# Kernel tuning notes

Hardware: AMD Instinct MI355X
Metric: run time of the kernel (lower is better)

Reference implementation:

```python
import jax, jax.numpy as jnp
import numpy as np

B, N, IN_C = 8, 2048, 256
HEADS, OUT_C = 4, 128
E = 65536
BN_EPS = 1e-5


def setup_inputs() -> dict:
    key = jax.random.key(0)
    k1, k2, k3, k4 = jax.random.split(key, 4)
    x = jax.random.normal(k1, (B, N, IN_C), dtype=jnp.float32)
    edge_index = jax.random.randint(k2, (2, E), 0, N, dtype=jnp.int64)
    # Linear W: in_channels -> heads*out_channels, no bias (stored as [in, out])
    W = jax.random.normal(k3, (IN_C, HEADS * OUT_C), dtype=jnp.float32) / np.sqrt(IN_C)
    # att Linear: 2*out_channels -> 1, no bias (stored as a vector)
    a = jax.random.normal(k4, (2 * OUT_C,), dtype=jnp.float32) / np.sqrt(2 * OUT_C)
    bn_gamma = jnp.ones((OUT_C,), dtype=jnp.float32)
    bn_beta = jnp.zeros((OUT_C,), dtype=jnp.float32)
    return {"x": x, "edge_index": edge_index, "W": W, "a": a,
            "bn_gamma": bn_gamma, "bn_beta": bn_beta}


def reference(x, edge_index, W, a, bn_gamma, bn_beta):
    Bsz, Nn, _ = x.shape
    src, dst = edge_index[0], edge_index[1]
    h = (x @ W).reshape(Bsz, Nn, HEADS, OUT_C)  # [B,N,H,C]
    # att([h_src, h_dst]) == h_src @ a[:C] + h_dst @ a[C:] ; precompute per node
    s_src = jnp.einsum("bnhc,c->bnh", h, a[:OUT_C])  # [B,N,H]
    s_dst = jnp.einsum("bnhc,c->bnh", h, a[OUT_C:])
    e = s_src[:, src] + s_dst[:, dst]                 # [B,E,H]
    e = jax.nn.leaky_relu(e, negative_slope=0.2)
    e_avg = e.mean(axis=-1)                           # [B,E]
    # dense N x N attention: rows = dst, cols = src, -inf elsewhere
    attn = jnp.full((Bsz, Nn, Nn), -jnp.inf, dtype=x.dtype)
    attn = attn.at[:, dst, src].set(e_avg)
    attn = jax.nn.softmax(attn, axis=-1)
    attn = jnp.nan_to_num(attn, nan=0.0)              # rows with no edges -> 0
    # dropout is identity in eval mode
    h_flat = h.reshape(Bsz, Nn, HEADS * OUT_C)
    h_out = attn @ h_flat                             # [B,N,H*C]
    h_out = h_out.reshape(Bsz, Nn, HEADS, OUT_C).mean(axis=2)  # [B,N,C]
    # BatchNorm1d over channel dim (batch stats, biased var, affine params)
    mean = h_out.mean(axis=(0, 1))
    var = h_out.var(axis=(0, 1))
    h_out = (h_out - mean) / jnp.sqrt(var + BN_EPS) * bn_gamma + bn_beta
    return jax.nn.elu(h_out)
```

## Files before the change

kernel.cpp:

```cpp
#include <hip/hip_runtime.h>
#include <hip/hip_bf16.h>
#include <math.h>

#define BB 8
#define NN 2048
#define INC 256
#define CC 128
#define NE 65536
#define CAP 128
#define MROWS (BB*NN)
#define BN_EPS 1e-5f
#define NT 9
#define NKC 8
#define NFRAG (NT*NKC*64)
#define FPSCALE 4194304.0

typedef unsigned int uint32;
typedef unsigned long long u64;
typedef __attribute__((ext_vector_type(8))) short short8;
typedef __attribute__((ext_vector_type(4))) float f32x4;

__device__ inline ushort f2bf(float f) {
  __hip_bfloat16 b = __float2bfloat16(f);
  return reinterpret_cast<ushort&>(b);
}
__device__ inline float bf2f(ushort h) {
  return __uint_as_float(((uint32)h) << 16);
}

__device__ inline void load_edge(const void* ei, int is64, int e, int& s, int& d) {
  if (is64) {
    const long long* p = (const long long*)ei;
    s = (int)p[e]; d = (int)p[NE + e];
  } else {
    const int* p = (const int*)ei;
    s = p[e]; d = p[NE + e];
  }
}

__global__ __launch_bounds__(256) void k_prep(const float* __restrict__ W,
                                              const float* __restrict__ a,
                                              const int* __restrict__ ei32,
                                              uint4* __restrict__ pack,
                                              int* __restrict__ flag,
                                              int* __restrict__ row_cnt,
                                              u64* __restrict__ bins) {
  __shared__ float Wl[8][520];
  __shared__ float Wms[8][132];
  __shared__ float Was[8][8];
  __shared__ float av[256];
  int m = blockIdx.x, tid = threadIdx.x;
  if (m < 8) row_cnt[m * 256 + tid] = 0;
  if (m == 8) {
    #pragma unroll
    for (int i = 0; i < 8; ++i) bins[tid * 8 + i] = 0ull;
  }
  if (m == 0 && tid == 0) {
    int nz = 0;
    for (int t = 1; t < 128; t += 2) nz |= (ei32[t] != 0);
    *flag = nz ? 0 : 1;
  }
  av[tid] = a[tid];
  const float4* Wg = (const float4*)(W + (size_t)m * 8 * 512);
  #pragma unroll
  for (int i = 0; i < 4; ++i) {
    int idx = tid + i * 256;
    int r = idx >> 7, c4 = idx & 127;
    *(float4*)&Wl[r][c4 * 4] = Wg[idx];
  }
  __syncthreads();
  {
    int c = tid & 127, half = tid >> 7;
    #pragma unroll
    for (int ii = 0; ii < 4; ++ii) {
      int r = half * 4 + ii;
      Wms[r][c] = 0.25f * (Wl[r][c] + Wl[r][128 + c] + Wl[r][256 + c] + Wl[r][384 + c]);
    }
  }
  {
    int i8 = tid >> 5, c2 = tid & 31;
    float p[8];
    #pragma unroll
    for (int j = 0; j < 8; ++j) p[j] = 0.0f;
    #pragma unroll
    for (int t4 = 0; t4 < 4; ++t4) {
      int cc = c2 + t4 * 32;
      float asrc = av[cc], adst = av[128 + cc];
      #pragma unroll
      for (int h = 0; h < 4; ++h) {
        float w = Wl[i8][h * 128 + cc];
        p[h] += w * asrc;
        p[4 + h] += w * adst;
      }
    }
    #pragma unroll
    for (int off = 16; off > 0; off >>= 1)
      #pragma unroll
      for (int j = 0; j < 8; ++j) p[j] += __shfl_xor(p[j], off, 64);
    if (c2 < 8) Was[i8][c2] = p[c2];
  }
  __syncthreads();
  if (tid < 144) {
    int t = tid >> 4, l16 = tid & 15;
    int cch = t * 16 + l16;
    int kc = m >> 2, g = m & 3;
    uint32 h[8];
    #pragma unroll
    for (int j = 0; j < 8; ++j) {
      float v = 0.0f;
      if (cch < CC) v = Wms[j][cch];
      else if (cch < CC + 8) v = Was[j][cch - CC];
      h[j] = (uint32)f2bf(v);
    }
    uint4 u;
    u.x = h[0] | (h[1] << 16);
    u.y = h[2] | (h[3] << 16);
    u.z = h[4] | (h[5] << 16);
    u.w = h[6] | (h[7] << 16);
    pack[(t * NKC + kc) * 64 + g * 16 + l16] = u;
  }
}

__global__ __launch_bounds__(512) void k_gemm(const float* __restrict__ x,
                                              const uint4* __restrict__ pack,
                                              const void* __restrict__ ei,
                                              const int* __restrict__ flag,
                                              ushort* __restrict__ hm,
                                              float* __restrict__ s,
                                              int* __restrict__ row_cnt,
                                              int* __restrict__ row_src) {
  __shared__ uint4 lp[NFRAG];
  int tid = threadIdx.x;
  if (tid < 256) {
    int e = blockIdx.x * 256 + tid;
    int is64 = *flag;
    int src, dst;
    load_edge(ei, is64, e, src, dst);
    int pos = atomicAdd(&row_cnt[dst], 1);
    if (pos < CAP) row_src[dst * CAP + pos] = src;
  }
  #pragma unroll
  for (int i = 0; i < 9; ++i) lp[i * 512 + tid] = pack[i * 512 + tid];

  int lane = tid & 63, wv = tid >> 6;
  int rt = wv & 3, th = wv >> 2;
  int g = lane >> 4;
  int xrow = blockIdx.x * 64 + rt * 16 + (lane & 15);
  const float* xr = x + (size_t)xrow * INC;

  short8 xf[8];
  #pragma unroll
  for (int kc = 0; kc < 8; ++kc) {
    f32x4 xa = *(const f32x4*)(xr + kc * 32 + g * 8);
    f32x4 xb = *(const f32x4*)(xr + kc * 32 + g * 8 + 4);
    short8 t;
    t[0] = (short)f2bf(xa[0]); t[1] = (short)f2bf(xa[1]);
    t[2] = (short)f2bf(xa[2]); t[3] = (short)f2bf(xa[3]);
    t[4] = (short)f2bf(xb[0]); t[5] = (short)f2bf(xb[1]);
    t[6] = (short)f2bf(xb[2]); t[7] = (short)f2bf(xb[3]);
    xf[kc] = t;
  }
  __syncthreads();

  f32x4 acc[4];
  f32x4 accE = (f32x4)(0.0f);
  #pragma unroll
  for (int i = 0; i < 4; ++i) acc[i] = (f32x4)(0.0f);

  const short8* fr = (const short8*)lp;
  int tb = th * 4;
  #pragma unroll
  for (int kc = 0; kc < NKC; ++kc) {
    #pragma unroll
    for (int i = 0; i < 4; ++i) {
      short8 af = fr[((tb + i) * NKC + kc) * 64 + lane];
      acc[i] = __builtin_amdgcn_mfma_f32_16x16x32_bf16(af, xf[kc], acc[i], 0, 0, 0);
    }
    short8 ae = fr[(8 * NKC + kc) * 64 + lane];
    accE = __builtin_amdgcn_mfma_f32_16x16x32_bf16(ae, xf[kc], accE, 0, 0, 0);
  }

  ushort* hrow = hm + (size_t)xrow * CC;
  #pragma unroll
  for (int i = 0; i < 4; ++i) {
    int t = tb + i;
    uint32 p0 = (uint32)f2bf(acc[i][0]) | ((uint32)f2bf(acc[i][1]) << 16);
    uint32 p1 = (uint32)f2bf(acc[i][2]) | ((uint32)f2bf(acc[i][3]) << 16);
    *(uint2*)(hrow + t * 16 + g * 4) = make_uint2(p0, p1);
  }
  if (th == 1 && g < 2) {
    *(f32x4*)(s + (size_t)xrow * 8 + g * 4) = accE;
  }
}

__device__ inline float edge_e(f32x4 ss, f32x4 sd) {
  float sum = 0.0f;
  #pragma unroll
  for (int h = 0; h < 4; ++h) {
    float v = ss[h] + sd[h];
    sum += (v > 0.0f) ? v : 0.2f * v;
  }
  return 0.25f * sum;
}

__global__ __launch_bounds__(256) void k_agg(const int* __restrict__ row_cnt,
                                             const int* __restrict__ row_src,
                                             const float* __restrict__ s,
                                             const uint32* __restrict__ hm32,
                                             uint32* __restrict__ hout,
                                             u64* __restrict__ bins) {
  __shared__ int rsrc[CAP], csrc[CAP];
  __shared__ float swgt[8][CAP];
  __shared__ f32x4 red[256];
  __shared__ uint32 bmask[64];
  __shared__ int wcnt[2];
  int d = blockIdx.x, tid = threadIdx.x;
  int lane = tid & 63, wv = tid >> 6;
  int k0 = row_cnt[d]; if (k0 > CAP) k0 = CAP;

  if (tid < 64) bmask[tid] = 0u;
  if (tid < k0) rsrc[tid] = row_src[d * CAP + tid];
  __syncthreads();
  int keep = 0;
  if (tid < k0) {
    int sv = rsrc[tid];
    uint32 bit = 1u << (sv & 31);
    uint32 old = atomicOr(&bmask[sv >> 5], bit);
    keep = ((old & bit) == 0) ? 1 : 0;
  }
  u64 mask = __ballot(keep);
  int pos = __popcll(mask & ((1ull << lane) - 1ull));
  if (lane == 0 && wv < 2) wcnt[wv] = (int)__popcll(mask);
  __syncthreads();
  int base = (wv == 1) ? wcnt[0] : 0;
  if (keep) csrc[base + pos] = rsrc[tid];
  __syncthreads();
  int kd = wcnt[0] + wcnt[1];
  if (tid < kd) {
    int sv = csrc[tid], r = 0;
    for (int q = 0; q < kd; ++q) r += (csrc[q] < sv) ? 1 : 0;
    rsrc[r] = sv;
  }
  __syncthreads();

  int b0 = wv, b1 = wv + 4;
  const float* sb0 = s + (size_t)b0 * NN * 8;
  const float* sb1 = s + (size_t)b1 * NN * 8;
  f32x4 sd0 = *(const f32x4*)(sb0 + (size_t)d * 8 + 4);
  f32x4 sd1 = *(const f32x4*)(sb1 + (size_t)d * 8 + 4);
  float v00 = -INFINITY, v01 = -INFINITY, v10 = -INFINITY, v11 = -INFINITY;
  if (lane < kd) {
    int r = rsrc[lane];
    f32x4 s0 = *(const f32x4*)(sb0 + (size_t)r * 8);
    f32x4 s1 = *(const f32x4*)(sb1 + (size_t)r * 8);
    v00 = edge_e(s0, sd0);
    v10 = edge_e(s1, sd1);
  }
  if (lane + 64 < kd) {
    int r = rsrc[lane + 64];
    f32x4 s0 = *(const f32x4*)(sb0 + (size_t)r * 8);
    f32x4 s1 = *(const f32x4*)(sb1 + (size_t)r * 8);
    v01 = edge_e(s0, sd0);
    v11 = edge_e(s1, sd1);
  }
  float m0 = fmaxf(v00, v01), m1 = fmaxf(v10, v11);
  #pragma unroll
  for (int off = 32; off > 0; off >>= 1) {
    m0 = fmaxf(m0, __shfl_xor(m0, off, 64));
    m1 = fmaxf(m1, __shfl_xor(m1, off, 64));
  }
  float e00 = (lane < kd)      ? expf(v00 - m0) : 0.0f;
  float e01 = (lane + 64 < kd) ? expf(v01 - m0) : 0.0f;
  float e10 = (lane < kd)      ? expf(v10 - m1) : 0.0f;
  float e11 = (lane + 64 < kd) ? expf(v11 - m1) : 0.0f;
  float sum0 = e00 + e01, sum1 = e10 + e11;
  #pragma unroll
  for (int off = 32; off > 0; off >>= 1) {
    sum0 += __shfl_xor(sum0, off, 64);
    sum1 += __shfl_xor(sum1, off, 64);
  }
  float inv0 = (kd > 0) ? 1.0f / sum0 : 0.0f;
  float inv1 = (kd > 0) ? 1.0f / sum1 : 0.0f;
  swgt[b0][lane]      = e00 * inv0;
  swgt[b0][lane + 64] = e01 * inv0;
  swgt[b1][lane]      = e10 * inv1;
  swgt[b1][lane + 64] = e11 * inv1;

  float a0 = 0.0f, a1 = 0.0f, a2 = 0.0f, a3 = 0.0f;
  const uint32* hb0 = hm32 + (size_t)b0 * NN * (CC / 2);
  const uint32* hb1 = hm32 + (size_t)b1 * NN * (CC / 2);
  #pragma unroll 4
  for (int j = 0; j < kd; ++j) {
    int r = rsrc[j];
    float w0 = swgt[b0][j], w1 = swgt[b1][j];
    uint32 u0 = hb0[(size_t)r * (CC / 2) + lane];
    uint32 u1 = hb1[(size_t)r * (CC / 2) + lane];
    a0 += w0 * bf2f((ushort)(u0 & 0xffffu));
    a1 += w0 * bf2f((ushort)(u0 >> 16));
    a2 += w1 * bf2f((ushort)(u1 & 0xffffu));
    a3 += w1 * bf2f((ushort)(u1 >> 16));
  }
  hout[((size_t)b0 * NN + d) * (CC / 2) + lane] =
      (uint32)f2bf(a0) | ((uint32)f2bf(a1) << 16);
  hout[((size_t)b1 * NN + d) * (CC / 2) + lane] =
      (uint32)f2bf(a2) | ((uint32)f2bf(a3) << 16);

  f32x4 r4;
  r4[0] = a0 + a2; r4[1] = a0 * a0 + a2 * a2;
  r4[2] = a1 + a3; r4[3] = a1 * a1 + a3 * a3;
  red[tid] = r4;
  __syncthreads();
  if (wv == 0) {
    f32x4 t = red[lane] + red[lane + 64] + red[lane + 128] + red[lane + 192];
    u64* bb = bins + (size_t)(d & 7) * (CC * 2);
    atomicAdd(&bb[4 * lane + 0], (u64)(long long)llrint((double)t[0] * FPSCALE));
    atomicAdd(&bb[4 * lane + 1], (u64)(long long)llrint((double)t[1] * FPSCALE));
    atomicAdd(&bb[4 * lane + 2], (u64)(long long)llrint((double)t[2] * FPSCALE));
    atomicAdd(&bb[4 * lane + 3], (u64)(long long)llrint((double)t[3] * FPSCALE));
  }
}

__global__ __launch_bounds__(256) void k_elu(const uint32* __restrict__ hout,
                                             const u64* __restrict__ bins,
                                             const float* __restrict__ gamma,
                                             const float* __restrict__ beta,
                                             float* __restrict__ out) {
  __shared__ float bsc[CC], bsh[CC];
  int tid = threadIdx.x;
  if (tid < CC) {
    long long S = 0, Q = 0;
    #pragma unroll
    for (int bin = 0; bin < 8; ++bin) {
      S += (long long)bins[bin * (CC * 2) + 2 * tid];
      Q += (long long)bins[bin * (CC * 2) + 2 * tid + 1];
    }
    double mean = (double)S / FPSCALE / (double)MROWS;
    double var  = (double)Q / FPSCALE / (double)MROWS - mean * mean;
    if (var < 0.0) var = 0.0;
    float scale = gamma[tid] / sqrtf((float)var + BN_EPS);
    bsc[tid] = scale;
    bsh[tid] = beta[tid] - (float)mean * scale;
  }
  __syncthreads();
  int pbase = blockIdx.x * 1024 + tid;
  #pragma unroll
  for (int i = 0; i < 4; ++i) {
    int p = pbase + i * 256;
    int cp = p & 63;
    uint32 u = hout[p];
    float y0 = bf2f((ushort)(u & 0xffffu)) * bsc[2 * cp]     + bsh[2 * cp];
    float y1 = bf2f((ushort)(u >> 16))     * bsc[2 * cp + 1] + bsh[2 * cp + 1];
    float2 o;
    o.x = (y0 > 0.0f) ? y0 : expm1f(y0);
    o.y = (y1 > 0.0f) ? y1 : expm1f(y1);
    *(float2*)(out + 2 * (size_t)p) = o;
  }
}

extern "C" void kernel_launch(void* const* d_in, const int* in_sizes, int n_in,
                              void* d_out, int out_size, void* d_ws, size_t ws_size,
                              hipStream_t stream) {
  const float* x     = (const float*)d_in[0];
  const void*  ei    = d_in[1];
  const float* W     = (const float*)d_in[2];
  const float* a     = (const float*)d_in[3];
  const float* gamma = (const float*)d_in[4];
  const float* beta  = (const float*)d_in[5];
  float* out = (float*)d_out;

  char* p = (char*)d_ws;
  ushort* hm   = (ushort*)p; p += (size_t)MROWS * CC * 2;
  uint32* hout = (uint32*)p; p += (size_t)MROWS * CC * 2;
  float* s    = (float*)p; p += (size_t)MROWS * 8 * 4;
  uint4* pack = (uint4*)p; p += (size_t)NFRAG * 16;
  u64* bins   = (u64*)p;   p += 8 * CC * 2 * 8;
  int* flag   = (int*)p;   p += 256;
  int* row_cnt  = (int*)p; p += NN * 4;
  int* row_src  = (int*)p; p += (size_t)NN * CAP * 4;

  k_prep<<<32, 256, 0, stream>>>(W, a, (const int*)ei, pack, flag, row_cnt, bins);
  k_gemm<<<MROWS / 64, 512, 0, stream>>>(x, pack, ei, flag, hm, s, row_cnt, row_src);
  k_agg<<<NN, 256, 0, stream>>>(row_cnt, row_src, s, (const uint32*)hm, hout, bins);
  k_elu<<<(MROWS * CC / 2) / 1024, 256, 0, stream>>>(hout, bins, gamma, beta, out);
}
```

Before: 63.32 us.

## Interleave batch pairs in projected features for wider gathers and packed FMA

The GEMM now writes its bf16 output so that batch b and batch b+4 share the same node row, stored as interleaved 32-bit words. The aggregation kernel can then fetch both batches' features for a neighbour with one 8-byte load per lane instead of two 4-byte loads. It also stores the two batches' softmax weights as a float2 pair and accumulates with two-wide float vectors, which can map to packed FMA instructions. The cost is strided 32-bit stores in the GEMM epilogue instead of contiguous 8-byte stores, and correctness depends on the aggregation's wave-to-batch mapping being b0=wv, b1=wv+4.

```diff
diff --git a/kernel.cpp b/kernel.cpp
--- a/kernel.cpp
+++ b/kernel.cpp
@@ -19,6 +19,7 @@
 typedef unsigned long long u64;
 typedef __attribute__((ext_vector_type(8))) short short8;
 typedef __attribute__((ext_vector_type(4))) float f32x4;
+typedef __attribute__((ext_vector_type(2))) float f32x2;
 
 __device__ inline ushort f2bf(float f) {
   __hip_bfloat16 b = __float2bfloat16(f);
@@ -125,7 +126,7 @@
                                               const uint4* __restrict__ pack,
                                               const void* __restrict__ ei,
                                               const int* __restrict__ flag,
-                                              ushort* __restrict__ hm,
+                                              uint32* __restrict__ hm32,
                                               float* __restrict__ s,
                                               int* __restrict__ row_cnt,
                                               int* __restrict__ row_src) {
@@ -180,13 +181,16 @@
     accE = __builtin_amdgcn_mfma_f32_16x16x32_bf16(ae, xf[kc], accE, 0, 0, 0);
   }
 
-  ushort* hrow = hm + (size_t)xrow * CC;
+  int b = xrow >> 11, n = xrow & (NN - 1);
+  int pp = b & 3, hh = b >> 2;
+  uint32* hbase = hm32 + ((size_t)pp * NN + n) * 128 + hh;
   #pragma unroll
   for (int i = 0; i < 4; ++i) {
     int t = tb + i;
     uint32 p0 = (uint32)f2bf(acc[i][0]) | ((uint32)f2bf(acc[i][1]) << 16);
     uint32 p1 = (uint32)f2bf(acc[i][2]) | ((uint32)f2bf(acc[i][3]) << 16);
-    *(uint2*)(hrow + t * 16 + g * 4) = make_uint2(p0, p1);
+    hbase[(t * 8 + g * 2) * 2]     = p0;
+    hbase[(t * 8 + g * 2 + 1) * 2] = p1;
   }
   if (th == 1 && g < 2) {
     *(f32x4*)(s + (size_t)xrow * 8 + g * 4) = accE;
@@ -206,11 +210,11 @@
 __global__ __launch_bounds__(256) void k_agg(const int* __restrict__ row_cnt,
                                              const int* __restrict__ row_src,
                                              const float* __restrict__ s,
-                                             const uint32* __restrict__ hm32,
+                                             const uint2* __restrict__ hm2,
                                              uint32* __restrict__ hout,
                                              u64* __restrict__ bins) {
   __shared__ int rsrc[CAP], csrc[CAP];
-  __shared__ float swgt[8][CAP];
+  __shared__ float2 swp[4][CAP];
   __shared__ f32x4 red[256];
   __shared__ uint32 bmask[64];
   __shared__ int wcnt[2];
@@ -281,33 +285,33 @@
   }
   float inv0 = (kd > 0) ? 1.0f / sum0 : 0.0f;
   float inv1 = (kd > 0) ? 1.0f / sum1 : 0.0f;
-  swgt[b0][lane]      = e00 * inv0;
-  swgt[b0][lane + 64] = e01 * inv0;
-  swgt[b1][lane]      = e10 * inv1;
-  swgt[b1][lane + 64] = e11 * inv1;
-
-  float a0 = 0.0f, a1 = 0.0f, a2 = 0.0f, a3 = 0.0f;
-  const uint32* hb0 = hm32 + (size_t)b0 * NN * (CC / 2);
-  const uint32* hb1 = hm32 + (size_t)b1 * NN * (CC / 2);
-  #pragma unroll 4
+  swp[wv][lane]      = make_float2(e00 * inv0, e10 * inv1);
+  swp[wv][lane + 64] = make_float2(e01 * inv0, e11 * inv1);
+
+  f32x2 a01 = (f32x2)(0.0f);
+  f32x2 a23 = (f32x2)(0.0f);
+  const uint2* hp = hm2 + (size_t)wv * NN * 64 + lane;
+  #pragma unroll 8
   for (int j = 0; j < kd; ++j) {
     int r = rsrc[j];
-    float w0 = swgt[b0][j], w1 = swgt[b1][j];
-    uint32 u0 = hb0[(size_t)r * (CC / 2) + lane];
-    uint32 u1 = hb1[(size_t)r * (CC / 2) + lane];
-    a0 += w0 * bf2f((ushort)(u0 & 0xffffu));
-    a1 += w0 * bf2f((ushort)(u0 >> 16));
-    a2 += w1 * bf2f((ushort)(u1 & 0xffffu));
-    a3 += w1 * bf2f((ushort)(u1 >> 16));
+    float2 w = swp[wv][j];
+    uint2 u = hp[(size_t)r * 64];
+    f32x2 h0, h1;
+    h0[0] = __uint_as_float(u.x << 16);
+    h0[1] = __uint_as_float(u.x & 0xffff0000u);
+    h1[0] = __uint_as_float(u.y << 16);
+    h1[1] = __uint_as_float(u.y & 0xffff0000u);
+    a01 += h0 * w.x;
+    a23 += h1 * w.y;
   }
   hout[((size_t)b0 * NN + d) * (CC / 2) + lane] =
-      (uint32)f2bf(a0) | ((uint32)f2bf(a1) << 16);
+      (uint32)f2bf(a01[0]) | ((uint32)f2bf(a01[1]) << 16);
   hout[((size_t)b1 * NN + d) * (CC / 2) + lane] =
-      (uint32)f2bf(a2) | ((uint32)f2bf(a3) << 16);
+      (uint32)f2bf(a23[0]) | ((uint32)f2bf(a23[1]) << 16);
 
   f32x4 r4;
-  r4[0] = a0 + a2; r4[1] = a0 * a0 + a2 * a2;
-  r4[2] = a1 + a3; r4[3] = a1 * a1 + a3 * a3;
+  r4[0] = a01[0] + a23[0]; r4[1] = a01[0] * a01[0] + a23[0] * a23[0];
+  r4[2] = a01[1] + a23[1]; r4[3] = a01[1] * a01[1] + a23[1] * a23[1];
   red[tid] = r4;
   __syncthreads();
   if (wv == 0) {
@@ -369,7 +373,7 @@
   float* out = (float*)d_out;
 
   char* p = (char*)d_ws;
-  ushort* hm   = (ushort*)p; p += (size_t)MROWS * CC * 2;
+  uint32* hm  = (uint32*)p; p += (size_t)MROWS * CC * 2;
   uint32* hout = (uint32*)p; p += (size_t)MROWS * CC * 2;
   float* s    = (float*)p; p += (size_t)MROWS * 8 * 4;
   uint4* pack = (uint4*)p; p += (size_t)NFRAG * 16;
@@ -380,6 +384,6 @@
 
   k_prep<<<32, 256, 0, stream>>>(W, a, (const int*)ei, pack, flag, row_cnt, bins);
   k_gemm<<<MROWS / 64, 512, 0, stream>>>(x, pack, ei, flag, hm, s, row_cnt, row_src);
-  k_agg<<<NN, 256, 0, stream>>>(row_cnt, row_src, s, (const uint32*)hm, hout, bins);
+  k_agg<<<NN, 256, 0, stream>>>(row_cnt, row_src, s, (const uint2*)hm, hout, bins);
   k_elu<<<(MROWS * CC / 2) / 1024, 256, 0, stream>>>(hout, bins, gamma, beta, out);
 }
```

Measured after the change: 69.01 us. 9.0% more time.

## Interleave score layout by batch, share edge scores, replace BN atomics with reduction kernel

Applied to the files above, without the earlier changes.

Stores the per-node attention scores node-major with batch interleaved, so one gather per source node fetches all eight batches contiguously. Edge logits for all batches are computed cooperatively into shared memory, replacing per-wave scattered loads. The 64-bit fixed-point atomic BatchNorm statistics are replaced by per-row partial sums written to a buffer and reduced in a new small kernel. This adds an extra launch and switches the statistics to float sums, which may change rounding slightly.

```diff
diff --git a/kernel.cpp b/kernel.cpp
--- a/kernel.cpp
+++ b/kernel.cpp
@@ -13,7 +13,6 @@
 #define NT 9
 #define NKC 8
 #define NFRAG (NT*NKC*64)
-#define FPSCALE 4194304.0
 
 typedef unsigned int uint32;
 typedef unsigned long long u64;
@@ -43,18 +42,13 @@
                                               const int* __restrict__ ei32,
                                               uint4* __restrict__ pack,
                                               int* __restrict__ flag,
-                                              int* __restrict__ row_cnt,
-                                              u64* __restrict__ bins) {
+                                              int* __restrict__ row_cnt) {
   __shared__ float Wl[8][520];
   __shared__ float Wms[8][132];
   __shared__ float Was[8][8];
   __shared__ float av[256];
   int m = blockIdx.x, tid = threadIdx.x;
   if (m < 8) row_cnt[m * 256 + tid] = 0;
-  if (m == 8) {
-    #pragma unroll
-    for (int i = 0; i < 8; ++i) bins[tid * 8 + i] = 0ull;
-  }
   if (m == 0 && tid == 0) {
     int nz = 0;
     for (int t = 1; t < 128; t += 2) nz |= (ei32[t] != 0);
@@ -189,18 +183,9 @@
     *(uint2*)(hrow + t * 16 + g * 4) = make_uint2(p0, p1);
   }
   if (th == 1 && g < 2) {
-    *(f32x4*)(s + (size_t)xrow * 8 + g * 4) = accE;
-  }
-}
-
-__device__ inline float edge_e(f32x4 ss, f32x4 sd) {
-  float sum = 0.0f;
-  #pragma unroll
-  for (int h = 0; h < 4; ++h) {
-    float v = ss[h] + sd[h];
-    sum += (v > 0.0f) ? v : 0.2f * v;
-  }
-  return 0.25f * sum;
+    int b = xrow >> 11, n = xrow & (NN - 1);
+    *(f32x4*)(s + ((size_t)n * BB + b) * 8 + g * 4) = accE;
+  }
 }
 
 __global__ __launch_bounds__(256) void k_agg(const int* __restrict__ row_cnt,
@@ -208,9 +193,11 @@
                                              const float* __restrict__ s,
                                              const uint32* __restrict__ hm32,
                                              uint32* __restrict__ hout,
-                                             u64* __restrict__ bins) {
+                                             f32x4* __restrict__ part) {
   __shared__ int rsrc[CAP], csrc[CAP];
   __shared__ float swgt[8][CAP];
+  __shared__ float emat[8][CAP];
+  __shared__ float sdl[8][4];
   __shared__ f32x4 red[256];
   __shared__ uint32 bmask[64];
   __shared__ int wcnt[2];
@@ -219,6 +206,10 @@
   int k0 = row_cnt[d]; if (k0 > CAP) k0 = CAP;
 
   if (tid < 64) bmask[tid] = 0u;
+  if (tid < 32) {
+    int b = tid >> 2, h = tid & 3;
+    sdl[b][h] = s[((size_t)d * BB + b) * 8 + 4 + h];
+  }
   if (tid < k0) rsrc[tid] = row_src[d * CAP + tid];
   __syncthreads();
   int keep = 0;
@@ -243,26 +234,30 @@
   }
   __syncthreads();
 
+  {
+    int jj = tid >> 3, bb = tid & 7;
+    for (int j0 = 0; j0 < kd; j0 += 32) {
+      int j = j0 + jj;
+      if (j < kd) {
+        int r = rsrc[j];
+        f32x4 ss = *(const f32x4*)(s + ((size_t)r * BB + bb) * 8);
+        float sum = 0.0f;
+        #pragma unroll
+        for (int h = 0; h < 4; ++h) {
+          float v = ss[h] + sdl[bb][h];
+          sum += (v > 0.0f) ? v : 0.2f * v;
+        }
+        emat[bb][j] = 0.25f * sum;
+      }
+    }
+  }
+  __syncthreads();
+
   int b0 = wv, b1 = wv + 4;
-  const float* sb0 = s + (size_t)b0 * NN * 8;
-  const float* sb1 = s + (size_t)b1 * NN * 8;
-  f32x4 sd0 = *(const f32x4*)(sb0 + (size_t)d * 8 + 4);
-  f32x4 sd1 = *(const f32x4*)(sb1 + (size_t)d * 8 + 4);
-  float v00 = -INFINITY, v01 = -INFINITY, v10 = -INFINITY, v11 = -INFINITY;
-  if (lane < kd) {
-    int r = rsrc[lane];
-    f32x4 s0 = *(const f32x4*)(sb0 + (size_t)r * 8);
-    f32x4 s1 = *(const f32x4*)(sb1 + (size_t)r * 8);
-    v00 = edge_e(s0, sd0);
-    v10 = edge_e(s1, sd1);
-  }
-  if (lane + 64 < kd) {
-    int r = rsrc[lane + 64];
-    f32x4 s0 = *(const f32x4*)(sb0 + (size_t)r * 8);
-    f32x4 s1 = *(const f32x4*)(sb1 + (size_t)r * 8);
-    v01 = edge_e(s0, sd0);
-    v11 = edge_e(s1, sd1);
-  }
+  float v00 = (lane < kd)      ? emat[b0][lane]      : -INFINITY;
+  float v01 = (lane + 64 < kd) ? emat[b0][lane + 64] : -INFINITY;
+  float v10 = (lane < kd)      ? emat[b1][lane]      : -INFINITY;
+  float v11 = (lane + 64 < kd) ? emat[b1][lane + 64] : -INFINITY;
   float m0 = fmaxf(v00, v01), m1 = fmaxf(v10, v11);
   #pragma unroll
   for (int off = 32; off > 0; off >>= 1) {
@@ -312,34 +307,49 @@
   __syncthreads();
   if (wv == 0) {
     f32x4 t = red[lane] + red[lane + 64] + red[lane + 128] + red[lane + 192];
-    u64* bb = bins + (size_t)(d & 7) * (CC * 2);
-    atomicAdd(&bb[4 * lane + 0], (u64)(long long)llrint((double)t[0] * FPSCALE));
-    atomicAdd(&bb[4 * lane + 1], (u64)(long long)llrint((double)t[1] * FPSCALE));
-    atomicAdd(&bb[4 * lane + 2], (u64)(long long)llrint((double)t[2] * FPSCALE));
-    atomicAdd(&bb[4 * lane + 3], (u64)(long long)llrint((double)t[3] * FPSCALE));
+    part[(size_t)d * 64 + lane] = t;
+  }
+}
+
+__global__ __launch_bounds__(256) void k_bnred(const f32x4* __restrict__ part,
+                                               const float* __restrict__ gamma,
+                                               const float* __restrict__ beta,
+                                               float* __restrict__ bntab) {
+  __shared__ f32x4 red[256];
+  int c = blockIdx.x, t = threadIdx.x;
+  f32x4 acc = (f32x4)(0.0f);
+  #pragma unroll
+  for (int i = 0; i < 8; ++i)
+    acc += part[(size_t)(t + 256 * i) * 64 + c];
+  red[t] = acc;
+  __syncthreads();
+  for (int off = 128; off > 0; off >>= 1) {
+    if (t < off) red[t] += red[t + off];
+    __syncthreads();
+  }
+  if (t == 0) {
+    f32x4 v = red[0];
+    #pragma unroll
+    for (int i = 0; i < 2; ++i) {
+      int ch = 2 * c + i;
+      float mean = v[2 * i] / (float)MROWS;
+      float var  = v[2 * i + 1] / (float)MROWS - mean * mean;
+      if (var < 0.0f) var = 0.0f;
+      float scale = gamma[ch] / sqrtf(var + BN_EPS);
+      bntab[ch] = scale;
+      bntab[CC + ch] = beta[ch] - mean * scale;
+    }
   }
 }
 
 __global__ __launch_bounds__(256) void k_elu(const uint32* __restrict__ hout,
-                                             const u64* __restrict__ bins,
-                                             const float* __restrict__ gamma,
-                                             const float* __restrict__ beta,
+                                             const float* __restrict__ bntab,
                                              float* __restrict__ out) {
   __shared__ float bsc[CC], bsh[CC];
   int tid = threadIdx.x;
   if (tid < CC) {
-    long long S = 0, Q = 0;
-    #pragma unroll
-    for (int bin = 0; bin < 8; ++bin) {
-      S += (long long)bins[bin * (CC * 2) + 2 * tid];
-      Q += (long long)bins[bin * (CC * 2) + 2 * tid + 1];
-    }
-    double mean = (double)S / FPSCALE / (double)MROWS;
-    double var  = (double)Q / FPSCALE / (double)MROWS - mean * mean;
-    if (var < 0.0) var = 0.0;
-    float scale = gamma[tid] / sqrtf((float)var + BN_EPS);
-    bsc[tid] = scale;
-    bsh[tid] = beta[tid] - (float)mean * scale;
+    bsc[tid] = bntab[tid];
+    bsh[tid] = bntab[CC + tid];
   }
   __syncthreads();
   int pbase = blockIdx.x * 1024 + tid;
@@ -371,15 +381,17 @@
   char* p = (char*)d_ws;
   ushort* hm   = (ushort*)p; p += (size_t)MROWS * CC * 2;
   uint32* hout = (uint32*)p; p += (size_t)MROWS * CC * 2;
+  f32x4* part = (f32x4*)p; p += (size_t)NN * 64 * 16;
   float* s    = (float*)p; p += (size_t)MROWS * 8 * 4;
   uint4* pack = (uint4*)p; p += (size_t)NFRAG * 16;
-  u64* bins   = (u64*)p;   p += 8 * CC * 2 * 8;
+  float* bntab = (float*)p; p += 4096;
   int* flag   = (int*)p;   p += 256;
   int* row_cnt  = (int*)p; p += NN * 4;
   int* row_src  = (int*)p; p += (size_t)NN * CAP * 4;
 
-  k_prep<<<32, 256, 0, stream>>>(W, a, (const int*)ei, pack, flag, row_cnt, bins);
+  k_prep<<<32, 256, 0, stream>>>(W, a, (const int*)ei, pack, flag, row_cnt);
   k_gemm<<<MROWS / 64, 512, 0, stream>>>(x, pack, ei, flag, hm, s, row_cnt, row_src);
-  k_agg<<<NN, 256, 0, stream>>>(row_cnt, row_src, s, (const uint32*)hm, hout, bins);
-  k_elu<<<(MROWS * CC / 2) / 1024, 256, 0, stream>>>(hout, bins, gamma, beta, out);
-}
+  k_agg<<<NN, 256, 0, stream>>>(row_cnt, row_src, s, (const uint32*)hm, hout, part);
+  k_bnred<<<64, 256, 0, stream>>>(part, gamma, beta, bntab);
+  k_elu<<<(MROWS * CC / 2) / 1024, 256, 0, stream>>>(hout, bntab, out);
+}
```

Measured after the change: 53.94 us. 1.17x faster.
